# Kernel optimization log

Measured on AMD Instinct MI355X. Metric: run time of the kernel, lower is better.

## Reference

```python
import jax, jax.numpy as jnp
import numpy as np

FEAT = 64
K = 16
K4 = K // 4
EPS = 1e-5  # BatchNorm eps (inference mode with running stats)


def _conv1x1(x, w, b):
    # x: (B, Cin, N, K), w: (Cout, Cin), b: (Cout,)
    return jnp.einsum('oc,bcnk->bonk', w, x) + b[None, :, None, None]


def _bn(x, g, be, m, v):
    # inference-mode BatchNorm2d over channel axis 1
    inv = g / jnp.sqrt(v + EPS)
    return (x - m[None, :, None, None]) * inv[None, :, None, None] + be[None, :, None, None]


def setup_inputs() -> dict:
    key = jax.random.key(0)
    ks = jax.random.split(key, 20)
    B, N, M = 4, 8192, 8192
    d = {}
    d['original_pts'] = jax.random.normal(ks[0], (B, 3, M), dtype=jnp.float32)
    d['query_pts'] = jax.random.normal(ks[1], (B, 3, N), dtype=jnp.float32)
    d['local_feat'] = jax.random.normal(ks[2], (B, FEAT, M), dtype=jnp.float32)
    # mlp_0: Conv2D(3, FEAT) with BN + ReLU
    d['w0'] = jax.random.normal(ks[3], (FEAT, 3), dtype=jnp.float32) * 0.2
    d['b0'] = jax.random.normal(ks[4], (FEAT,), dtype=jnp.float32) * 0.01
    d['g0'] = 1.0 + 0.1 * jax.random.normal(ks[5], (FEAT,), dtype=jnp.float32)
    d['be0'] = 0.01 * jax.random.normal(ks[6], (FEAT,), dtype=jnp.float32)
    d['m0'] = 0.01 * jax.random.normal(ks[7], (FEAT,), dtype=jnp.float32)
    d['v0'] = jax.random.uniform(ks[8], (FEAT,), dtype=jnp.float32, minval=0.5, maxval=1.5)
    # mlp_1: Conv2D(FEAT, FEAT) with BN + ReLU
    d['w1'] = jax.random.normal(ks[9], (FEAT, FEAT), dtype=jnp.float32) * 0.1
    d['b1'] = jax.random.normal(ks[10], (FEAT,), dtype=jnp.float32) * 0.01
    d['g1'] = 1.0 + 0.1 * jax.random.normal(ks[11], (FEAT,), dtype=jnp.float32)
    d['be1'] = 0.01 * jax.random.normal(ks[12], (FEAT,), dtype=jnp.float32)
    d['m1'] = 0.01 * jax.random.normal(ks[13], (FEAT,), dtype=jnp.float32)
    d['v1'] = jax.random.uniform(ks[14], (FEAT,), dtype=jnp.float32, minval=0.5, maxval=1.5)
    # mlp_2: Conv2D(2*FEAT, 1), no BN, no ReLU
    d['w2'] = jax.random.normal(ks[15], (1, 2 * FEAT), dtype=jnp.float32) * 0.1
    d['b2'] = jax.random.normal(ks[16], (1,), dtype=jnp.float32) * 0.01
    return d


def reference(original_pts, query_pts, local_feat,
              w0, b0, g0, be0, m0, v0,
              w1, b1, g1, be1, m1, v1,
              w2, b2):
    B, _, N = query_pts.shape
    # --- KNN: squared distances (B, N, M), take K smallest ---
    q2 = jnp.sum(query_pts ** 2, axis=1)          # (B, N)
    o2 = jnp.sum(original_pts ** 2, axis=1)       # (B, M)
    cross = jnp.einsum('bcn,bcm->bnm', query_pts, original_pts)
    d2 = q2[:, :, None] + o2[:, None, :] - 2.0 * cross
    _, knn_idx = jax.lax.top_k(-d2, K)            # (B, N, K)

    # gather neighbor coords: (B, 3, N, K)
    knn_pts = jax.vmap(lambda pts, idx: pts[:, idx])(original_pts, knn_idx)
    # gather local features for first K//4 neighbors: (B, FEAT, N, K4)
    patch_feat = jax.vmap(lambda f, idx: f[:, idx])(local_feat, knn_idx[:, :, :K4])

    relative_pts = knn_pts - query_pts[:, :, :, None]  # (B, 3, N, K)
    feat0 = jax.nn.relu(_bn(_conv1x1(relative_pts, w0, b0), g0, be0, m0, v0))  # (B, F, N, K)
    feat_g = jnp.max(feat0, axis=3, keepdims=True)                              # (B, F, N, 1)
    relative_feat = jax.nn.relu(_bn(_conv1x1(feat0, w1, b1), g1, be1, m1, v1))[:, :, :, :K4]
    feat2 = jnp.concatenate(
        [relative_feat, jnp.broadcast_to(feat_g, (B, FEAT, N, K4))], axis=1)    # (B, 2F, N, K4)
    weight = jax.nn.sigmoid(_conv1x1(feat2, w2, b2))                            # (B, 1, N, K4)
    query_feat = (1.0 - weight) * relative_feat + weight * patch_feat
    return jnp.sum(query_feat, axis=-1)  # (B, FEAT, N)
```

## Files before the change

### kernel.cpp

```cpp
#include <hip/hip_runtime.h>
#include <cstdint>

#define M_PTS 8192
#define N_QRY 8192
#define BATCH 4

__device__ __forceinline__ float d2_exact(float qx, float qy, float qz, float q2, float4 p) {
#pragma clang fp contract(off)
  float dot = (qx * p.x + qy * p.y) + qz * p.z;
  return (q2 + p.w) - 2.0f * dot;
}

__device__ __forceinline__ unsigned flipf(float d) {
  unsigned u = __float_as_uint(d);
  return u ^ ((unsigned)((int)u >> 31) | 0x80000000u);
}

__device__ __forceinline__ int lane_prefix(unsigned long long m) {
  return __builtin_amdgcn_mbcnt_hi((unsigned)(m >> 32),
         __builtin_amdgcn_mbcnt_lo((unsigned)m, 0));
}

__device__ __forceinline__ void ld_lds16(const float4* g, float4* l) {
  __builtin_amdgcn_global_load_lds((const __attribute__((address_space(1))) void*)g,
                                   (__attribute__((address_space(3))) void*)l, 16, 0, 0);
}

__device__ __forceinline__ float tau16(float mn) {
  float lo = mn, hi = mn;
#pragma unroll
  for (int j = 1; j < 64; j <<= 1) {
    lo = fminf(lo, __shfl_xor(lo, j));
    hi = fmaxf(hi, __shfl_xor(hi, j));
  }
#pragma unroll
  for (int it = 0; it < 12; it++) {
    float mid = 0.5f * (lo + hi);
    int cnt = __popcll(__ballot(mn <= mid));
    if (cnt >= 16) hi = mid; else lo = mid;
  }
  return hi;
}

__global__ void pack_pts(const float* __restrict__ src, float4* __restrict__ dst, int total) {
#pragma clang fp contract(off)
  int i = blockIdx.x * 256 + threadIdx.x;
  if (i >= total) return;
  int b = i >> 13, m = i & (M_PTS - 1);
  const float* s = src + (size_t)b * 3 * M_PTS;
  float x = s[m], y = s[M_PTS + m], z = s[2 * M_PTS + m];
  float ss = (x * x + y * y) + z * z;
  dst[i] = make_float4(x, y, z, ss);
}

__global__ void transpose_lf(const float* __restrict__ lf, float* __restrict__ lfT) {
  __shared__ float tile[64][65];
  int bb = blockIdx.x >> 7;
  int m0 = (blockIdx.x & 127) << 6;
  int tm = threadIdx.x & 63;
  int tc = threadIdx.x >> 6;
  const float* src = lf + (size_t)bb * 64 * M_PTS;
#pragma unroll
  for (int i = 0; i < 16; i++) {
    int ch = i * 4 + tc;
    tile[ch][tm] = src[(size_t)ch * M_PTS + m0 + tm];
  }
  __syncthreads();
  float* dst = lfT + ((size_t)bb * M_PTS + m0) * 64;
#pragma unroll
  for (int i = 0; i < 16; i++) {
    int mm = i * 4 + tc;
    dst[(size_t)mm * 64 + tm] = tile[tm][mm];
  }
}

__global__ void __launch_bounds__(256, 4) knn_kernel(const float4* __restrict__ pp,
                                                     const float4* __restrict__ qp,
                                                     int* __restrict__ knn_out) {
  __shared__ float4 spts[2048];
  __shared__ unsigned cand[8][192];
  const int tid = threadIdx.x;
  const int lane = tid & 63;
  const int wave = tid >> 6;
  const int b = blockIdx.x >> 10;
  const int qa = blockIdx.x * 8 + wave * 2;
  const float4* pb = pp + ((size_t)b << 13);

  const float4 A4 = qp[qa];
  const float4 B4 = qp[qa + 1];
  const float axA = -2.0f * A4.x, ayA = -2.0f * A4.y, azA = -2.0f * A4.z;
  const float axB = -2.0f * B4.x, ayB = -2.0f * B4.y, azB = -2.0f * B4.z;

  int cntA = 0, cntB = 0;
  unsigned* cqA = cand[wave * 2 + 0];
  unsigned* cqB = cand[wave * 2 + 1];

  for (int c = 0; c < 4; ++c) {
    __syncthreads();
#pragma unroll
    for (int i = 0; i < 8; i++) {
      const float4* g = pb + c * 2048 + i * 256 + wave * 64 + lane;
      ld_lds16(g, &spts[i * 256 + wave * 64]);
    }
    __syncthreads();

    float eA[32], eB[32];
    float mnA = 3.402823466e38f, mnB = 3.402823466e38f;
#pragma unroll
    for (int j = 0; j < 32; j++) {
      float4 p = spts[j * 64 + lane];
      float ea = __builtin_fmaf(axA, p.x, __builtin_fmaf(ayA, p.y,
                 __builtin_fmaf(azA, p.z, p.w)));
      float eb = __builtin_fmaf(axB, p.x, __builtin_fmaf(ayB, p.y,
                 __builtin_fmaf(azB, p.z, p.w)));
      eA[j] = ea;
      eB[j] = eb;
      mnA = fminf(mnA, ea);
      mnB = fminf(mnB, eb);
    }
    float tauA = tau16(mnA) + 0.01f;
    float tauB = tau16(mnB) + 0.01f;

#pragma unroll
    for (int j = 0; j < 32; j++) {
      unsigned idx = (unsigned)(c * 2048 + j * 64 + lane);
      {
        bool pred = eA[j] <= tauA;
        unsigned long long mask = __ballot(pred);
        if (mask) {
          int pos = cntA + lane_prefix(mask);
          if (pred && pos < 192) cqA[pos] = idx;
          cntA += __popcll(mask);
        }
      }
      {
        bool pred = eB[j] <= tauB;
        unsigned long long mask = __ballot(pred);
        if (mask) {
          int pos = cntB + lane_prefix(mask);
          if (pred && pos < 192) cqB[pos] = idx;
          cntB += __popcll(mask);
        }
      }
    }
  }

  auto finalize = [&](const unsigned* cq, int cnt, int gq,
                      float qx, float qy, float qz, float q2) {
    int E = cnt < 192 ? cnt : 192;
    unsigned i0 = (lane < E) ? cq[lane] : 0u;
    unsigned i1 = (lane + 64 < E) ? cq[lane + 64] : 0u;
    unsigned i2 = (lane + 128 < E) ? cq[lane + 128] : 0u;
    float4 p0 = pb[i0];
    float4 p1 = pb[i1];
    float4 p2 = pb[i2];
    unsigned long long k0 = ~0ull, k1 = ~0ull, k2 = ~0ull;
    if (lane < E)
      k0 = ((unsigned long long)flipf(d2_exact(qx, qy, qz, q2, p0)) << 32) | i0;
    if (lane + 64 < E)
      k1 = ((unsigned long long)flipf(d2_exact(qx, qy, qz, q2, p1)) << 32) | i1;
    if (lane + 128 < E)
      k2 = ((unsigned long long)flipf(d2_exact(qx, qy, qz, q2, p2)) << 32) | i2;
    unsigned my = 0;
#pragma unroll
    for (int t = 0; t < 16; t++) {
      unsigned long long m = k0 < k1 ? k0 : k1;
      if (k2 < m) m = k2;
#pragma unroll
      for (int j = 1; j < 64; j <<= 1) {
        unsigned long long o = __shfl_xor(m, j);
        if (o < m) m = o;
      }
      if (lane == t) my = (unsigned)m;
      if (k0 == m) k0 = ~0ull;
      else if (k1 == m) k1 = ~0ull;
      else if (k2 == m) k2 = ~0ull;
    }
    if (lane < 16) knn_out[(size_t)gq * 16 + lane] = (int)my;
  };

  finalize(cqA, cntA, qa,     A4.x, A4.y, A4.z, A4.w);
  finalize(cqB, cntB, qa + 1, B4.x, B4.y, B4.z, B4.w);
}

__global__ void __launch_bounds__(256, 3) feat_kernel(
    const float4* __restrict__ pp, const float4* __restrict__ qp,
    const int* __restrict__ knn, const float* __restrict__ lfT,
    const float* __restrict__ w0, const float* __restrict__ b0,
    const float* __restrict__ g0, const float* __restrict__ be0,
    const float* __restrict__ m0, const float* __restrict__ v0,
    const float* __restrict__ w1, const float* __restrict__ b1,
    const float* __restrict__ g1, const float* __restrict__ be1,
    const float* __restrict__ m1, const float* __restrict__ v1,
    const float* __restrict__ w2, const float* __restrict__ b2,
    float* __restrict__ out) {
  __shared__ float4 relbuf[4][16];
  __shared__ float4 f0v[4][64];
  __shared__ float outbuf[64][17];
  const int tid = threadIdx.x;
  const int lane = tid & 63;
  const int wave = tid >> 6;
  const int gq0 = blockIdx.x * 16;
  const int b = gq0 >> 13;

  const float inv0 = g0[lane] / sqrtf(v0[lane] + 1e-5f);
  const float w00 = w0[lane * 3 + 0] * inv0;
  const float w01 = w0[lane * 3 + 1] * inv0;
  const float w02 = w0[lane * 3 + 2] * inv0;
  const float bb0 = (b0[lane] - m0[lane]) * inv0 + be0[lane];
  const float inv1 = g1[lane] / sqrtf(v1[lane] + 1e-5f);
  const float bb1 = (b1[lane] - m1[lane]) * inv1 + be1[lane];

  float w1s[64];
#pragma unroll
  for (int i = 0; i < 16; i++) {
    float4 t = ((const float4*)(w1 + (size_t)lane * 64))[i];
    w1s[i * 4 + 0] = t.x; w1s[i * 4 + 1] = t.y;
    w1s[i * 4 + 2] = t.z; w1s[i * 4 + 3] = t.w;
  }
  const float w2a = w2[lane], w2b = w2[64 + lane];
  const float bias2 = b2[0];
  const float4* pb = pp + ((size_t)b << 13);
  const float* lfb = lfT + (((size_t)b << 13)) * 64;

  for (int qi = 0; qi < 4; qi++) {
    const int gq = gq0 + wave * 4 + qi;
    const float4 q4 = qp[gq];
    int nk = knn[(size_t)gq * 16 + (lane & 15)];
    float4 pk = pb[nk];
    if (lane < 16)
      relbuf[wave][lane] = make_float4(pk.x - q4.x, pk.y - q4.y, pk.z - q4.z, 0.0f);

    float g = 0.0f, f0 = 0, f1 = 0, f2 = 0, f3 = 0;
#pragma unroll
    for (int k = 0; k < 16; k++) {
      float4 r = relbuf[wave][k];
      float y = fmaxf(0.0f, w00 * r.x + w01 * r.y + w02 * r.z + bb0);
      g = fmaxf(g, y);
      if (k == 0) f0 = y; else if (k == 1) f1 = y;
      else if (k == 2) f2 = y; else if (k == 3) f3 = y;
    }
    f0v[wave][lane] = make_float4(f0, f1, f2, f3);

    float a0 = 0, a1 = 0, a2 = 0, a3 = 0;
#pragma unroll
    for (int c2 = 0; c2 < 64; c2++) {
      float w = w1s[c2];
      float4 fb = f0v[wave][c2];
      a0 = fmaf(w, fb.x, a0); a1 = fmaf(w, fb.y, a1);
      a2 = fmaf(w, fb.z, a2); a3 = fmaf(w, fb.w, a3);
    }
    float r0 = fmaxf(0.0f, fmaf(a0, inv1, bb1));
    float r1 = fmaxf(0.0f, fmaf(a1, inv1, bb1));
    float r2 = fmaxf(0.0f, fmaf(a2, inv1, bb1));
    float r3 = fmaxf(0.0f, fmaf(a3, inv1, bb1));

    int i0 = __shfl(nk, 0), i1 = __shfl(nk, 1), i2 = __shfl(nk, 2), i3 = __shfl(nk, 3);
    float p0 = lfb[(size_t)i0 * 64 + lane];
    float p1 = lfb[(size_t)i1 * 64 + lane];
    float p2 = lfb[(size_t)i2 * 64 + lane];
    float p3 = lfb[(size_t)i3 * 64 + lane];

    float s0 = w2a * r0, s1 = w2a * r1, s2 = w2a * r2, s3 = w2a * r3, tg = w2b * g;
#pragma unroll
    for (int j = 1; j < 64; j <<= 1) {
      s0 += __shfl_xor(s0, j);
      s1 += __shfl_xor(s1, j);
      s2 += __shfl_xor(s2, j);
      s3 += __shfl_xor(s3, j);
      tg += __shfl_xor(tg, j);
    }
    float wk0 = 1.0f / (1.0f + __expf(-(s0 + tg + bias2)));
    float wk1 = 1.0f / (1.0f + __expf(-(s1 + tg + bias2)));
    float wk2 = 1.0f / (1.0f + __expf(-(s2 + tg + bias2)));
    float wk3 = 1.0f / (1.0f + __expf(-(s3 + tg + bias2)));

    float oc = ((1.0f - wk0) * r0 + wk0 * p0)
             + ((1.0f - wk1) * r1 + wk1 * p1)
             + ((1.0f - wk2) * r2 + wk2 * p2)
             + ((1.0f - wk3) * r3 + wk3 * p3);
    outbuf[lane][wave * 4 + qi] = oc;
  }
  __syncthreads();

  int c = tid >> 2, j = tid & 3;
  float4 o4 = make_float4(outbuf[c][j * 4 + 0], outbuf[c][j * 4 + 1],
                          outbuf[c][j * 4 + 2], outbuf[c][j * 4 + 3]);
  *(float4*)(out + (((size_t)(b * 64 + c)) << 13) + (gq0 & (N_QRY - 1)) + j * 4) = o4;
}

extern "C" void kernel_launch(void* const* d_in, const int* in_sizes, int n_in,
                              void* d_out, int out_size, void* d_ws, size_t ws_size,
                              hipStream_t stream) {
  (void)in_sizes; (void)n_in; (void)out_size; (void)ws_size;
  const float* original_pts = (const float*)d_in[0];
  const float* query_pts   = (const float*)d_in[1];
  const float* local_feat  = (const float*)d_in[2];
  const float* w0 = (const float*)d_in[3];
  const float* b0 = (const float*)d_in[4];
  const float* g0 = (const float*)d_in[5];
  const float* be0 = (const float*)d_in[6];
  const float* m0 = (const float*)d_in[7];
  const float* v0 = (const float*)d_in[8];
  const float* w1 = (const float*)d_in[9];
  const float* b1 = (const float*)d_in[10];
  const float* g1 = (const float*)d_in[11];
  const float* be1 = (const float*)d_in[12];
  const float* m1 = (const float*)d_in[13];
  const float* v1 = (const float*)d_in[14];
  const float* w2 = (const float*)d_in[15];
  const float* b2 = (const float*)d_in[16];
  float* out = (float*)d_out;

  char* ws = (char*)d_ws;
  float4* pp  = (float4*)(ws);
  float4* qp  = (float4*)(ws + 524288);
  float*  lfT = (float*)(ws + 1048576);
  int*    knn = (int*)(ws + 9437184);

  pack_pts<<<128, 256, 0, stream>>>(original_pts, pp, BATCH * M_PTS);
  pack_pts<<<128, 256, 0, stream>>>(query_pts, qp, BATCH * N_QRY);
  transpose_lf<<<512, 256, 0, stream>>>(local_feat, lfT);
  knn_kernel<<<4096, 256, 0, stream>>>(pp, qp, knn);
  feat_kernel<<<2048, 256, 0, stream>>>(pp, qp, knn, lfT,
                                        w0, b0, g0, be0, m0, v0,
                                        w1, b1, g1, be1, m1, v1,
                                        w2, b2, out);
}
```

Before: 302.1 us.

## Stream KNN in smaller chunks with running threshold and raise occupancy

The KNN kernel now loads point chunks of 1024 instead of 2048, which halves LDS staging. It no longer stores per-chunk distance arrays in registers. Instead it collects candidates in a single pass against a running threshold, seeded from the first chunk and tightened after each later chunk. Bisection iterations drop from 12 to 10, and launch bounds rise on both kernels; in feat_kernel, asm barriers pin the w1 weights in registers. This cuts register and LDS pressure to raise occupancy. The risks are candidate overflow past 192 if the early thresholds are loose, and spills in feat_kernel.

```diff
diff --git a/kernel.cpp b/kernel.cpp
--- a/kernel.cpp
+++ b/kernel.cpp
@@ -34,7 +34,7 @@
     hi = fmaxf(hi, __shfl_xor(hi, j));
   }
 #pragma unroll
-  for (int it = 0; it < 12; it++) {
+  for (int it = 0; it < 10; it++) {
     float mid = 0.5f * (lo + hi);
     int cnt = __popcll(__ballot(mn <= mid));
     if (cnt >= 16) hi = mid; else lo = mid;
@@ -74,10 +74,10 @@
   }
 }
 
-__global__ void __launch_bounds__(256, 4) knn_kernel(const float4* __restrict__ pp,
+__global__ void __launch_bounds__(256, 7) knn_kernel(const float4* __restrict__ pp,
                                                      const float4* __restrict__ qp,
                                                      int* __restrict__ knn_out) {
-  __shared__ float4 spts[2048];
+  __shared__ float4 spts[1024];
   __shared__ unsigned cand[8][192];
   const int tid = threadIdx.x;
   const int lane = tid & 63;
@@ -95,53 +95,58 @@
   unsigned* cqA = cand[wave * 2 + 0];
   unsigned* cqB = cand[wave * 2 + 1];
 
-  for (int c = 0; c < 4; ++c) {
+  float mnA = 3.402823466e38f, mnB = 3.402823466e38f;
+  float tauA = 0.0f, tauB = 0.0f;
+
+  auto collect = [&](float e, float tau, unsigned* cq, int& cnt, unsigned idx) {
+    bool pred = e <= tau;
+    unsigned long long mask = __ballot(pred);
+    if (mask) {
+      int pos = cnt + lane_prefix(mask);
+      if (pred && pos < 192) cq[pos] = idx;
+      cnt += __popcll(mask);
+    }
+  };
+
+  for (int c = 0; c < 8; ++c) {
     __syncthreads();
 #pragma unroll
-    for (int i = 0; i < 8; i++) {
-      const float4* g = pb + c * 2048 + i * 256 + wave * 64 + lane;
+    for (int i = 0; i < 4; i++) {
+      const float4* g = pb + c * 1024 + i * 256 + wave * 64 + lane;
       ld_lds16(g, &spts[i * 256 + wave * 64]);
     }
     __syncthreads();
 
-    float eA[32], eB[32];
-    float mnA = 3.402823466e38f, mnB = 3.402823466e38f;
-#pragma unroll
-    for (int j = 0; j < 32; j++) {
+    if (c == 0) {
+#pragma unroll
+      for (int j = 0; j < 16; j++) {
+        float4 p = spts[j * 64 + lane];
+        mnA = fminf(mnA, __builtin_fmaf(axA, p.x, __builtin_fmaf(ayA, p.y,
+                         __builtin_fmaf(azA, p.z, p.w))));
+        mnB = fminf(mnB, __builtin_fmaf(axB, p.x, __builtin_fmaf(ayB, p.y,
+                         __builtin_fmaf(azB, p.z, p.w))));
+      }
+      tauA = tau16(mnA) + 0.01f;
+      tauB = tau16(mnB) + 0.01f;
+    }
+
+#pragma unroll
+    for (int j = 0; j < 16; j++) {
       float4 p = spts[j * 64 + lane];
       float ea = __builtin_fmaf(axA, p.x, __builtin_fmaf(ayA, p.y,
                  __builtin_fmaf(azA, p.z, p.w)));
       float eb = __builtin_fmaf(axB, p.x, __builtin_fmaf(ayB, p.y,
                  __builtin_fmaf(azB, p.z, p.w)));
-      eA[j] = ea;
-      eB[j] = eb;
       mnA = fminf(mnA, ea);
       mnB = fminf(mnB, eb);
-    }
-    float tauA = tau16(mnA) + 0.01f;
-    float tauB = tau16(mnB) + 0.01f;
-
-#pragma unroll
-    for (int j = 0; j < 32; j++) {
-      unsigned idx = (unsigned)(c * 2048 + j * 64 + lane);
-      {
-        bool pred = eA[j] <= tauA;
-        unsigned long long mask = __ballot(pred);
-        if (mask) {
-          int pos = cntA + lane_prefix(mask);
-          if (pred && pos < 192) cqA[pos] = idx;
-          cntA += __popcll(mask);
-        }
-      }
-      {
-        bool pred = eB[j] <= tauB;
-        unsigned long long mask = __ballot(pred);
-        if (mask) {
-          int pos = cntB + lane_prefix(mask);
-          if (pred && pos < 192) cqB[pos] = idx;
-          cntB += __popcll(mask);
-        }
-      }
+      unsigned idx = (unsigned)(c * 1024 + j * 64 + lane);
+      collect(ea, tauA, cqA, cntA, idx);
+      collect(eb, tauB, cqB, cntB, idx);
+    }
+
+    if (c > 0 && c < 7) {
+      tauA = fminf(tauA, tau16(mnA) + 0.01f);
+      tauB = fminf(tauB, tau16(mnB) + 0.01f);
     }
   }
 
@@ -183,7 +188,7 @@
   finalize(cqB, cntB, qa + 1, B4.x, B4.y, B4.z, B4.w);
 }
 
-__global__ void __launch_bounds__(256, 3) feat_kernel(
+__global__ void __launch_bounds__(256, 4) feat_kernel(
     const float4* __restrict__ pp, const float4* __restrict__ qp,
     const int* __restrict__ knn, const float* __restrict__ lfT,
     const float* __restrict__ w0, const float* __restrict__ b0,
@@ -218,6 +223,9 @@
     w1s[i * 4 + 0] = t.x; w1s[i * 4 + 1] = t.y;
     w1s[i * 4 + 2] = t.z; w1s[i * 4 + 3] = t.w;
   }
+#pragma unroll
+  for (int k = 0; k < 64; k++) asm volatile("" : "+v"(w1s[k]));
+
   const float w2a = w2[lane], w2b = w2[64 + lane];
   const float bias2 = b2[0];
   const float4* pb = pp + ((size_t)b << 13);
```

Measured after the change: 297.5 us. About the same (-1.5%).
